# Kernel optimization log

Hardware: AMD Instinct MI355X
Metric: run time of the kernel (lower is better)

Reference implementation:

```python
import jax, jax.numpy as jnp
import numpy as np

EPS = 1e-8


def setup_inputs() -> dict:
    key = jax.random.key(0)
    ks = jax.random.split(key, 7)
    S, B, E, D, A = 2048, 32, 1024, 1024, 1024
    return {
        "decoder_state": jax.random.normal(ks[0], (B, D), jnp.float32),
        "encoder_states": jax.random.normal(ks[1], (S, B, E), jnp.float32),
        "noise": jax.random.normal(ks[2], (S, B), jnp.float32),
        "W_dec": jax.random.normal(ks[3], (D, A), jnp.float32) * (D ** -0.5),
        "W_enc": jax.random.normal(ks[4], (E, A), jnp.float32) * (E ** -0.5),
        "b": jax.random.normal(ks[5], (A,), jnp.float32) * 0.02,
        "v": jax.random.normal(ks[6], (A,), jnp.float32) * (A ** -0.5),
    }


def reference(decoder_state, encoder_states, noise, W_dec, W_enc, b, v):
    S, B, E = encoder_states.shape
    # Additive (Bahdanau) monotonic energy: e_sb = v . tanh(W_d s + W_e h + b)
    dec_proj = decoder_state @ W_dec                         # [B, A]
    enc_proj = jnp.einsum("sbe,ea->sba", encoder_states, W_enc)  # [S, B, A]
    energy = jnp.einsum("sba,a->sb", jnp.tanh(enc_proj + dec_proj[None] + b), v)
    # p_choose with pre-sigmoid Gaussian noise (noise_avg=0, noise_var=1)
    p_choose = jax.nn.sigmoid(energy + noise)                # [S, B]

    # previous_attention is None -> one-hot at source position 0
    prev_attn = jnp.zeros((S, B), p_choose.dtype).at[0].set(1.0)

    # exclusive cumprod of (1 - p) along src dim
    cp = jnp.cumprod(1.0 - p_choose, axis=0)
    cumprod_one_minus_p = jnp.concatenate(
        [jnp.ones((1, B), p_choose.dtype), cp[:-1]], axis=0)
    denom = jnp.clip(cumprod_one_minus_p, EPS, 1.0)
    alpha = p_choose * cumprod_one_minus_p * jnp.cumsum(prev_attn / denom, axis=0)

    # mass preservation (no padding mask): dump residual mass on last frame
    residual = 1.0 - jnp.clip(jnp.sum(alpha[:-1], axis=0), 0.0, 1.0)
    alpha = alpha.at[-1].set(residual)

    beta = alpha  # hard monotonic attention: beta == alpha
    weighted_context = jnp.einsum("sbe,sb->be", encoder_states, beta)  # [B, E]
    return weighted_context, alpha
```

## Files before the change

### kernel.cpp

```cpp
#include <hip/hip_runtime.h>
#include <hip/hip_fp16.h>

#define S_DIM 2048
#define B_DIM 32
#define E_DIM 1024
#define A_DIM 1024
#define D_DIM 1024
#define M_DIM (S_DIM * B_DIM)

typedef _Float16 f16x8 __attribute__((ext_vector_type(8)));
typedef _Float16 f16x4 __attribute__((ext_vector_type(4)));
typedef float f32x4 __attribute__((ext_vector_type(4)));

#define OFF_ENC 0ull
#define OFF_WT  134217728ull
#define OFF_DP  (OFF_WT + 2097152ull)
#define OFF_EN  (OFF_DP + 131072ull)

__device__ inline void load_lds16(const void* g, void* l) {
    __builtin_amdgcn_global_load_lds((const __attribute__((address_space(1))) void*)g,
                                     (__attribute__((address_space(3))) void*)l, 16, 0, 0);
}

__global__ void convert_enc_kernel(const float4* __restrict__ in, f16x4* __restrict__ out) {
    int idx = blockIdx.x * 256 + threadIdx.x;
    float4 f = in[idx];
    f16x4 o = { (_Float16)f.x, (_Float16)f.y, (_Float16)f.z, (_Float16)f.w };
    out[idx] = o;
}

__global__ void transpose_wenc_kernel(const float* __restrict__ W, _Float16* __restrict__ WT) {
    __shared__ _Float16 tile[32][33];
    int a0 = blockIdx.x * 32, e0 = blockIdx.y * 32;
    int tx = threadIdx.x & 31, ty = threadIdx.x >> 5;
    #pragma unroll
    for (int i = 0; i < 32; i += 8)
        tile[ty + i][tx] = (_Float16)W[(size_t)(e0 + ty + i) * A_DIM + a0 + tx];
    __syncthreads();
    #pragma unroll
    for (int i = 0; i < 32; i += 8)
        WT[(size_t)(a0 + ty + i) * E_DIM + e0 + tx] = tile[tx][ty + i];
}

__global__ void decproj_kernel(const float* __restrict__ dec, const float* __restrict__ Wd,
                               const float* __restrict__ bias, float* __restrict__ dp) {
    int a = blockIdx.x * 256 + threadIdx.x;
    int b = blockIdx.y;
    float acc = bias[a];
    const float* dr = dec + (size_t)b * D_DIM;
    const float* wcol = Wd + a;
    #pragma unroll 8
    for (int d = 0; d < D_DIM; ++d)
        acc += dr[d] * wcol[(size_t)d * A_DIM];
    dp[(size_t)b * A_DIM + a] = acc;
}

__global__ __launch_bounds__(512, 2)
void energy_gemm_kernel(const _Float16* __restrict__ Af, const _Float16* __restrict__ Bt,
                        const float* __restrict__ dp, const float* __restrict__ v,
                        float* __restrict__ energy) {
    __shared__ alignas(16) _Float16 As[4][256 * 32];
    __shared__ alignas(16) _Float16 Bs[4][256 * 32];

    const int tid = threadIdx.x;
    const int wid = tid >> 6;
    const int lane = tid & 63;
    const int quad = lane >> 4;
    const int l15 = lane & 15;

    const int bid = blockIdx.x;
    const int xcd = bid & 7;
    const int local = bid >> 3;
    const int m0 = (xcd * 32 + (local >> 2)) * 256;
    const int n0 = (local & 3) * 256;

    const int wm = (wid >> 2) * 128;
    const int wn = (wid & 3) * 64;

    const int lr = lane >> 2;
    const int lc = (lane & 3) * 8;
    const _Float16* Ag = Af + (size_t)(m0 + wid * 16 + lr) * E_DIM + lc;
    const _Float16* Bg = Bt + (size_t)(n0 + wid * 16 + lr) * E_DIM + lc;

#define STAGE_A(u)                                                              \
    {                                                                           \
        load_lds16(Ag + (size_t)(u) * 32, &As[(u) & 3][wid * 512]);             \
        load_lds16(Ag + (size_t)128 * E_DIM + (size_t)(u) * 32,                 \
                   &As[(u) & 3][(wid + 8) * 512]);                              \
    }
#define STAGE_B(u)                                                              \
    {                                                                           \
        load_lds16(Bg + (size_t)(u) * 32, &Bs[(u) & 3][wid * 512]);             \
        load_lds16(Bg + (size_t)128 * E_DIM + (size_t)(u) * 32,                 \
                   &Bs[(u) & 3][(wid + 8) * 512]);                              \
    }

    f32x4 acc[8][4] = {};

    STAGE_A(0) STAGE_B(0)
    STAGE_A(1) STAGE_B(1)
    STAGE_A(2) STAGE_B(2)
    asm volatile("s_waitcnt vmcnt(8)" ::: "memory");
    __builtin_amdgcn_s_barrier();
    asm volatile("" ::: "memory");

    #pragma unroll
    for (int t = 0; t < 32; ++t) {
        const int slot = t & 3;
        f16x8 af[4], bf[4];

        #pragma unroll
        for (int j = 0; j < 4; ++j)
            bf[j] = *(const f16x8*)&Bs[slot][(wn + j * 16 + l15) * 32 + quad * 8];
        #pragma unroll
        for (int i = 0; i < 4; ++i)
            af[i] = *(const f16x8*)&As[slot][(wm + i * 16 + l15) * 32 + quad * 8];
        if (t < 29) STAGE_A(t + 3)
        asm volatile("" ::: "memory");
        __builtin_amdgcn_s_barrier();
        asm volatile("" ::: "memory");
        __builtin_amdgcn_s_setprio(1);
        #pragma unroll
        for (int i = 0; i < 4; ++i)
            #pragma unroll
            for (int j = 0; j < 4; ++j)
                acc[i][j] = __builtin_amdgcn_mfma_f32_16x16x32_f16(af[i], bf[j], acc[i][j], 0, 0, 0);
        __builtin_amdgcn_s_setprio(0);
        asm volatile("" ::: "memory");
        __builtin_amdgcn_s_barrier();
        asm volatile("" ::: "memory");

        #pragma unroll
        for (int i = 0; i < 4; ++i)
            af[i] = *(const f16x8*)&As[slot][(wm + 64 + i * 16 + l15) * 32 + quad * 8];
        if (t < 29) STAGE_B(t + 3)
        asm volatile("" ::: "memory");
        __builtin_amdgcn_s_barrier();
        asm volatile("" ::: "memory");
        __builtin_amdgcn_s_setprio(1);
        #pragma unroll
        for (int i = 0; i < 4; ++i)
            #pragma unroll
            for (int j = 0; j < 4; ++j)
                acc[4 + i][j] = __builtin_amdgcn_mfma_f32_16x16x32_f16(af[i], bf[j], acc[4 + i][j], 0, 0, 0);
        __builtin_amdgcn_s_setprio(0);
        if (t <= 28)      asm volatile("s_waitcnt vmcnt(8)" ::: "memory");
        else if (t == 29) asm volatile("s_waitcnt vmcnt(4)" ::: "memory");
        else if (t == 30) asm volatile("s_waitcnt vmcnt(0)" ::: "memory");
        asm volatile("" ::: "memory");
        __builtin_amdgcn_s_barrier();
        asm volatile("" ::: "memory");
    }
#undef STAGE_A
#undef STAGE_B

    float vf[4];
    #pragma unroll
    for (int j = 0; j < 4; ++j) vf[j] = v[n0 + wn + j * 16 + l15];

    #pragma unroll
    for (int i = 0; i < 8; ++i) {
        #pragma unroll
        for (int r = 0; r < 4; ++r) {
            int m = m0 + wm + i * 16 + quad * 4 + r;
            int bidx = m & 31;
            float sum = 0.f;
            #pragma unroll
            for (int j = 0; j < 4; ++j) {
                int a = n0 + wn + j * 16 + l15;
                float x = acc[i][j][r] + dp[bidx * A_DIM + a];
                float ex = __expf(2.f * x);
                float th = 1.f - 2.f * __builtin_amdgcn_rcpf(ex + 1.f);
                sum += th * vf[j];
            }
            sum += __shfl_xor(sum, 1);
            sum += __shfl_xor(sum, 2);
            sum += __shfl_xor(sum, 4);
            sum += __shfl_xor(sum, 8);
            if (l15 == 0) atomicAdd(&energy[bidx * S_DIM + (m >> 5)], sum);
        }
    }
}

__global__ void scan_alpha_kernel(const float* __restrict__ energy, const float* __restrict__ noise,
                                  float* __restrict__ alpha) {
    __shared__ float sc[256];
    __shared__ float red[256];
    const int b = blockIdx.x;
    const int t = threadIdx.x;
    float p[8], q[8];
    float prod = 1.f;
    #pragma unroll
    for (int k = 0; k < 8; ++k) {
        int s = t * 8 + k;
        float x = energy[b * S_DIM + s] + noise[s * B_DIM + b];
        p[k] = __builtin_amdgcn_rcpf(1.f + __expf(-x));
        q[k] = __builtin_amdgcn_rcpf(1.f + __expf(x));
        prod *= q[k];
    }
    sc[t] = prod;
    __syncthreads();
    for (int off = 1; off < 256; off <<= 1) {
        float mine = sc[t];
        float other = (t >= off) ? sc[t - off] : 1.f;
        __syncthreads();
        sc[t] = mine * other;
        __syncthreads();
    }
    float run = (t > 0) ? sc[t - 1] : 1.f;
    float lsum = 0.f;
    #pragma unroll
    for (int k = 0; k < 8; ++k) {
        int s = t * 8 + k;
        float al = p[k] * run;
        run *= q[k];
        if (s < S_DIM - 1) { alpha[s * B_DIM + b] = al; lsum += al; }
    }
    red[t] = lsum;
    __syncthreads();
    for (int off = 128; off > 0; off >>= 1) {
        if (t < off) red[t] += red[t + off];
        __syncthreads();
    }
    if (t == 0) {
        float tot = fminf(fmaxf(red[0], 0.f), 1.f);
        alpha[(S_DIM - 1) * B_DIM + b] = 1.f - tot;
    }
}

__global__ void wc_kernel(const _Float16* __restrict__ enc, const float* __restrict__ alpha,
                          float* __restrict__ wc) {
    __shared__ float red[128][8];
    const int b = blockIdx.y;
    const int t = threadIdx.x;
    const int e0 = (t & 127) * 8;
    const int half = t >> 7;
    int s = blockIdx.x * 128 + half;
    float acc[8] = {};
    for (int i = 0; i < 64; ++i, s += 2) {
        float al = alpha[s * B_DIM + b];
        f16x8 r = *(const f16x8*)&enc[((size_t)s * B_DIM + b) * E_DIM + e0];
        #pragma unroll
        for (int k = 0; k < 8; ++k) acc[k] += al * (float)r[k];
    }
    if (half) {
        #pragma unroll
        for (int k = 0; k < 8; ++k) red[t - 128][k] = acc[k];
    }
    __syncthreads();
    if (!half) {
        #pragma unroll
        for (int k = 0; k < 8; ++k)
            atomicAdd(&wc[b * E_DIM + e0 + k], acc[k] + red[t][k]);
    }
}

extern "C" void kernel_launch(void* const* d_in, const int* in_sizes, int n_in,
                              void* d_out, int out_size, void* d_ws, size_t ws_size,
                              hipStream_t stream) {
    const float* dec   = (const float*)d_in[0];
    const float* enc   = (const float*)d_in[1];
    const float* noise = (const float*)d_in[2];
    const float* Wd    = (const float*)d_in[3];
    const float* We    = (const float*)d_in[4];
    const float* bias  = (const float*)d_in[5];
    const float* v     = (const float*)d_in[6];

    char* ws = (char*)d_ws;
    _Float16* encf = (_Float16*)(ws + OFF_ENC);
    _Float16* wtf  = (_Float16*)(ws + OFF_WT);
    float* dp      = (float*)(ws + OFF_DP);
    float* energy  = (float*)(ws + OFF_EN);

    float* wc    = (float*)d_out;
    float* alpha = (float*)d_out + B_DIM * E_DIM;

    (void)hipMemsetAsync(wc, 0, B_DIM * E_DIM * sizeof(float), stream);
    (void)hipMemsetAsync(energy, 0, M_DIM * sizeof(float), stream);

    convert_enc_kernel<<<dim3(M_DIM * E_DIM / 4 / 256), 256, 0, stream>>>((const float4*)enc, (f16x4*)encf);
    transpose_wenc_kernel<<<dim3(32, 32), 256, 0, stream>>>(We, wtf);
    decproj_kernel<<<dim3(4, 32), 256, 0, stream>>>(dec, Wd, bias, dp);
    energy_gemm_kernel<<<dim3(1024), 512, 0, stream>>>(encf, wtf, dp, v, energy);
    scan_alpha_kernel<<<dim3(32), 256, 0, stream>>>(energy, noise, alpha);
    wc_kernel<<<dim3(16, 32), 256, 0, stream>>>(encf, alpha, wc);
}
```

Measured before the change: 669.0 us.

## Swizzle LDS tile layout in energy GEMM and restructure dec projection with split-K

The energy GEMM now XOR-swizzles the 16-byte column chunk per row, both when staging into LDS and when reading fragments, to reduce LDS bank conflicts on the MFMA operand reads. The decoder projection kernel is rewritten so each thread reuses each W_dec element across 8 batch rows, and the reduction dimension is split across 4 blocks that combine with atomicAdd. This needs an extra memset of dp and makes the summation order nondeterministic.

```diff
diff --git a/kernel.cpp b/kernel.cpp
--- a/kernel.cpp
+++ b/kernel.cpp
@@ -44,15 +44,23 @@
 
 __global__ void decproj_kernel(const float* __restrict__ dec, const float* __restrict__ Wd,
                                const float* __restrict__ bias, float* __restrict__ dp) {
-    int a = blockIdx.x * 256 + threadIdx.x;
-    int b = blockIdx.y;
-    float acc = bias[a];
-    const float* dr = dec + (size_t)b * D_DIM;
-    const float* wcol = Wd + a;
-    #pragma unroll 8
-    for (int d = 0; d < D_DIM; ++d)
-        acc += dr[d] * wcol[(size_t)d * A_DIM];
-    dp[(size_t)b * A_DIM + a] = acc;
+    const int t = threadIdx.x;
+    const int a = blockIdx.x * 64 + (t & 63);
+    const int bg = t >> 6;
+    const int d0 = blockIdx.y * 256;
+    float acc[8] = {};
+    #pragma unroll 4
+    for (int d = d0; d < d0 + 256; ++d) {
+        float w = Wd[(size_t)d * A_DIM + a];
+        #pragma unroll
+        for (int bi = 0; bi < 8; ++bi)
+            acc[bi] += dec[(size_t)(bg * 8 + bi) * D_DIM + d] * w;
+    }
+    #pragma unroll
+    for (int bi = 0; bi < 8; ++bi) {
+        float add = acc[bi] + (blockIdx.y == 0 ? bias[a] : 0.f);
+        atomicAdd(&dp[(size_t)(bg * 8 + bi) * A_DIM + a], add);
+    }
 }
 
 __global__ __launch_bounds__(512, 2)
@@ -67,6 +75,7 @@
     const int lane = tid & 63;
     const int quad = lane >> 4;
     const int l15 = lane & 15;
+    const int rsw = ((l15 >> 1) & 3);
 
     const int bid = blockIdx.x;
     const int xcd = bid & 7;
@@ -78,7 +87,7 @@
     const int wn = (wid & 3) * 64;
 
     const int lr = lane >> 2;
-    const int lc = (lane & 3) * 8;
+    const int lc = ((lane & 3) ^ ((lane >> 3) & 3)) * 8;
     const _Float16* Ag = Af + (size_t)(m0 + wid * 16 + lr) * E_DIM + lc;
     const _Float16* Bg = Bt + (size_t)(n0 + wid * 16 + lr) * E_DIM + lc;
 
@@ -111,10 +120,10 @@
 
         #pragma unroll
         for (int j = 0; j < 4; ++j)
-            bf[j] = *(const f16x8*)&Bs[slot][(wn + j * 16 + l15) * 32 + quad * 8];
-        #pragma unroll
-        for (int i = 0; i < 4; ++i)
-            af[i] = *(const f16x8*)&As[slot][(wm + i * 16 + l15) * 32 + quad * 8];
+            bf[j] = *(const f16x8*)&Bs[slot][(wn + j * 16 + l15) * 32 + (quad ^ rsw) * 8];
+        #pragma unroll
+        for (int i = 0; i < 4; ++i)
+            af[i] = *(const f16x8*)&As[slot][(wm + i * 16 + l15) * 32 + (quad ^ rsw) * 8];
         if (t < 29) STAGE_A(t + 3)
         asm volatile("" ::: "memory");
         __builtin_amdgcn_s_barrier();
@@ -132,7 +141,7 @@
 
         #pragma unroll
         for (int i = 0; i < 4; ++i)
-            af[i] = *(const f16x8*)&As[slot][(wm + 64 + i * 16 + l15) * 32 + quad * 8];
+            af[i] = *(const f16x8*)&As[slot][(wm + 64 + i * 16 + l15) * 32 + (quad ^ rsw) * 8];
         if (t < 29) STAGE_B(t + 3)
         asm volatile("" ::: "memory");
         __builtin_amdgcn_s_barrier();
@@ -276,11 +285,12 @@
     float* alpha = (float*)d_out + B_DIM * E_DIM;
 
     (void)hipMemsetAsync(wc, 0, B_DIM * E_DIM * sizeof(float), stream);
+    (void)hipMemsetAsync(dp, 0, B_DIM * A_DIM * sizeof(float), stream);
     (void)hipMemsetAsync(energy, 0, M_DIM * sizeof(float), stream);
 
     convert_enc_kernel<<<dim3(M_DIM * E_DIM / 4 / 256), 256, 0, stream>>>((const float4*)enc, (f16x4*)encf);
     transpose_wenc_kernel<<<dim3(32, 32), 256, 0, stream>>>(We, wtf);
-    decproj_kernel<<<dim3(4, 32), 256, 0, stream>>>(dec, Wd, bias, dp);
+    decproj_kernel<<<dim3(16, 4), 256, 0, stream>>>(dec, Wd, bias, dp);
     energy_gemm_kernel<<<dim3(1024), 512, 0, stream>>>(encf, wtf, dp, v, energy);
     scan_alpha_kernel<<<dim3(32), 256, 0, stream>>>(energy, noise, alpha);
     wc_kernel<<<dim3(16, 32), 256, 0, stream>>>(encf, alpha, wc);
```

Result: faster. 640.1 us (-4.3%).
